# Kernel tuning notes

Measured on AMD Instinct MI355X. Metric: run time of the kernel, lower is better.

## Reference

```python
import jax, jax.numpy as jnp
import numpy as np

H, KV, D, HID = 32, 8, 128, 4096
B, S = 1, 2048
ROPE_THETA = 10000.0


def setup_inputs() -> dict:
    key = jax.random.key(0)
    ks = jax.random.split(key, 5)
    std = 0.02
    return {
        "x": jax.random.normal(ks[0], (B, S, HID), jnp.float32),
        "Wq": jax.random.normal(ks[1], (H * D, HID), jnp.float32) * std,
        "Wk": jax.random.normal(ks[2], (KV * D, HID), jnp.float32) * std,
        "Wv": jax.random.normal(ks[3], (KV * D, HID), jnp.float32) * std,
        "Wo": jax.random.normal(ks[4], (HID, H * D), jnp.float32) * std,
    }


def _rope_cos_sin(seq_len, dim, dtype):
    inv_freq = 1.0 / (ROPE_THETA ** (jnp.arange(0, dim, 2, dtype=jnp.float32) / dim))
    t = jnp.arange(seq_len, dtype=jnp.float32)
    freqs = jnp.einsum("s,d->sd", t, inv_freq)          # [S, D/2]
    emb = jnp.concatenate([freqs, freqs], axis=-1)        # [S, D]
    return jnp.cos(emb).astype(dtype), jnp.sin(emb).astype(dtype)


def _rotate_half(x):
    x1, x2 = jnp.split(x, 2, axis=-1)
    return jnp.concatenate([-x2, x1], axis=-1)


def reference(x, Wq, Wk, Wv, Wo):
    Bx, Sx, _ = x.shape
    q = (x @ Wq.T).reshape(Bx, Sx, H, D).transpose(0, 2, 1, 3)    # [B,H,S,D]
    k = (x @ Wk.T).reshape(Bx, Sx, KV, D).transpose(0, 2, 1, 3)   # [B,KV,S,D]
    v = (x @ Wv.T).reshape(Bx, Sx, KV, D).transpose(0, 2, 1, 3)

    cos, sin = _rope_cos_sin(Sx, D, x.dtype)                       # [S,D]
    q = q * cos + _rotate_half(q) * sin
    k = k * cos + _rotate_half(k) * sin

    rep = H // KV
    k = jnp.repeat(k, rep, axis=1)                                 # [B,H,S,D]
    v = jnp.repeat(v, rep, axis=1)

    scale = 1.0 / jnp.sqrt(jnp.asarray(D, x.dtype))
    scores = jnp.einsum("bhqd,bhkd->bhqk", q, k) * scale           # [B,H,S,S]
    causal = jnp.tril(jnp.ones((Sx, Sx), dtype=bool))
    scores = jnp.where(causal, scores, jnp.asarray(-1e30, x.dtype))
    attn = jax.nn.softmax(scores, axis=-1)
    out = jnp.einsum("bhqk,bhkd->bhqd", attn, v)                   # [B,H,S,D]
    out = out.transpose(0, 2, 1, 3).reshape(Bx, Sx, H * D)
    return out @ Wo.T
```

## Files before the change

kernel.cpp:

```cpp
#include <hip/hip_runtime.h>

typedef unsigned short u16;
typedef unsigned int u32;

using f32x4  = __attribute__((ext_vector_type(4))) float;
using f32x16 = __attribute__((ext_vector_type(16))) float;
using bf16x8 = __attribute__((ext_vector_type(8))) __bf16;

#define S_LEN 2048
#define HID_DIM 4096
#define NH 32
#define NKV 8
#define HD 128
#define QKVN 6144

__device__ __forceinline__ u16 f2b(float f) {
  union { float f; u32 u; } v; v.f = f;
  u32 r = (v.u + 0x7FFFu + ((v.u >> 16) & 1u)) >> 16;
  return (u16)r;
}
__device__ __forceinline__ float b2f(u16 b) {
  union { u32 u; float f; } v; v.u = ((u32)b) << 16;
  return v.f;
}

__device__ __forceinline__ u32 cvtpk_bf16(float lo, float hi) {
  u32 r;
  asm("v_cvt_pk_bf16_f32 %0, %1, %2" : "=v"(r) : "v"(lo), "v"(hi));
  return r;
}
__device__ __forceinline__ void plane_swap(u32& a, u32& b) {
  asm volatile("v_permlane32_swap_b32 %0, %1" : "+v"(a), "+v"(b));
}

#define AS1 __attribute__((address_space(1)))
#define AS3 __attribute__((address_space(3)))
__device__ __forceinline__ void gl_lds16(const u16* g, u16* l) {
  __builtin_amdgcn_global_load_lds((const AS1 u32*)g, (AS3 u32*)l, 16, 0, 0);
}

#define SBAR  __builtin_amdgcn_s_barrier()
#define SCHED0 __builtin_amdgcn_sched_barrier(0)
#define LGKM0 do { asm volatile("s_waitcnt lgkmcnt(0)" ::: "memory"); } while (0)
#define PRIO1 __builtin_amdgcn_s_setprio(1)
#define PRIO0 __builtin_amdgcn_s_setprio(0)

template <int N> __device__ __forceinline__ void waitv() {
  if constexpr (N == 0)      asm volatile("s_waitcnt vmcnt(0)" ::: "memory");
  else if constexpr (N == 6) asm volatile("s_waitcnt vmcnt(6)" ::: "memory");
  else if constexpr (N == 7) asm volatile("s_waitcnt vmcnt(7)" ::: "memory");
  else                       asm volatile("s_waitcnt vmcnt(0)" ::: "memory");
  SCHED0;
}

__global__ void cast_kernel(const float* __restrict__ src, u16* __restrict__ dst, int n4) {
  int i = blockIdx.x * blockDim.x + threadIdx.x;
  int stride = gridDim.x * blockDim.x;
  for (; i < n4; i += stride) {
    float4 v = ((const float4*)src)[i];
    uint2 o;
    o.x = (u32)f2b(v.x) | ((u32)f2b(v.y) << 16);
    o.y = (u32)f2b(v.z) | ((u32)f2b(v.w) << 16);
    ((uint2*)dst)[i] = o;
  }
}

#define STAGE(DST, SRC, CH, LDK)                                   \
  _Pragma("unroll") for (int c = 0; c < (CH); ++c) {               \
    int d_ = c * 8192 + tid * 16;                                  \
    int rw_ = d_ >> 7;                                             \
    int cb_ = (d_ & 127) ^ ((rw_ & 7) << 4);                       \
    gl_lds16((SRC) + (size_t)rw_ * (LDK) + (cb_ >> 1), (DST) + (d_ >> 1)); \
  }


#define RDA(ABUF, MLO, KS)                                                    \
  _Pragma("unroll") for (int mm = 0; mm < 4; ++mm)                            \
    af[(MLO) + mm][KS] = *(const bf16x8*)((const char*)(ABUF) +               \
      (wmo + ((MLO) + mm) * 16 + lr) * 128 + (((((KS) << 2) | lg) ^ lr7) << 4));

#define RDB(BBUF, KS)                                                         \
  _Pragma("unroll") for (int nn = 0; nn < NF; ++nn)                           \
    bfr[nn][KS] = *(const bf16x8*)((const char*)(BBUF) +                      \
      (wno + nn * 16 + lr) * 128 + (((((KS) << 2) | lg) ^ lr7) << 4));

#define MFMA_Q(MLO, KS)                                                       \
  _Pragma("unroll") for (int mm = 0; mm < 4; ++mm)                            \
  _Pragma("unroll") for (int nn = 0; nn < NF; ++nn)                           \
    acc[(MLO) + mm][nn] = __builtin_amdgcn_mfma_f32_16x16x32_bf16(            \
        af[(MLO) + mm][KS], bfr[nn][KS], acc[(MLO) + mm][nn], 0, 0, 0);

template <int BN, int WN, int CBF>
__global__ __launch_bounds__(512, 2) void gemm8p(
    const u16* __restrict__ A, const u16* __restrict__ B, void* __restrict__ Cout,
    int M, int N, int K)
{
  constexpr int BM = 256;
  constexpr int NF = WN / 16;
  constexpr int LA = BM / 64;
  constexpr int LB = BN / 64;
  constexpr int LT = LA + LB;
  extern __shared__ __align__(16) u16 smem[];
  u16* const As0 = smem;
  u16* const Bs0 = smem + 2 * BM * 64;

  const int tid  = threadIdx.x;
  const int lane = tid & 63;
  const int wave = tid >> 6;
  const int lr  = lane & 15;
  const int lg  = lane >> 4;
  const int lr7 = lane & 7;

  const int nbx = N / BN;
  const int bid = blockIdx.x;
  const int cpx = gridDim.x >> 3;
  const int swz = (bid & 7) * cpx + (bid >> 3);
  const int bm = (swz / nbx) * BM;
  const int bn = (swz % nbx) * BN;
  const int wmo = (wave >> 2) * 128;
  const int wno = (wave & 3) * WN;

  const int NT = K >> 6;

  f32x4 acc[8][NF] = {};
  bf16x8 af[8][2], bfr[NF][2];

  const u16* aP = A + (size_t)bm * K;
  const u16* bP = B + (size_t)bn * K;

  STAGE(As0,           aP,      LA, K);
  STAGE(Bs0,           bP,      LB, K);
  STAGE(As0 + BM * 64, aP + 64, LA, K);
  STAGE(Bs0 + BN * 64, bP + 64, LB, K);
  waitv<LT>();
  SBAR; SCHED0;

  for (int t = 0; t < NT; ++t) {
    const int buf = t & 1;
    const u16* ab = As0 + buf * (BM * 64);
    const u16* bb = Bs0 + buf * (BN * 64);
    const bool st = (t + 2 < NT);

    RDA(ab, 0, 0); RDA(ab, 4, 0); RDB(bb, 0);
    MFMA_Q(0, 0); MFMA_Q(4, 0);
    RDA(ab, 0, 1); RDA(ab, 4, 1); RDB(bb, 1);
    MFMA_Q(0, 1); MFMA_Q(4, 1);

    LGKM0;
    SCHED0;
    SBAR;
    if (st) {
      STAGE(As0 + buf * (BM * 64), aP + (size_t)(t + 2) * 64, LA, K);
      STAGE(Bs0 + buf * (BN * 64), bP + (size_t)(t + 2) * 64, LB, K);
    }
    if (t + 1 < NT) {
      if (st) waitv<LT>(); else waitv<0>();
    }
    SBAR; SCHED0;
  }

#pragma unroll
  for (int m = 0; m < 8; ++m)
#pragma unroll
    for (int j = 0; j < 4; ++j) {
      int row = bm + wmo + m * 16 + lg * 4 + j;
      size_t base = (size_t)row * N + bn + wno + lr;
      if constexpr (CBF) {
        u16* C = (u16*)Cout;
#pragma unroll
        for (int nn = 0; nn < NF; ++nn) C[base + nn * 16] = f2b(acc[m][nn][j]);
      } else {
        float* C = (float*)Cout;
#pragma unroll
        for (int nn = 0; nn < NF; ++nn) C[base + nn * 16] = acc[m][nn][j];
      }
    }
}

__global__ void rope_qk(const u16* __restrict__ qkv, u16* __restrict__ dst,
                        int col_off, float scale, int frag) {
  int idx = blockIdx.x * blockDim.x + threadIdx.x;
  int i = idx & 63;
  int s = (idx >> 6) & (S_LEN - 1);
  int h = idx >> 17;
  const u16* row = qkv + (size_t)s * QKVN + col_off + h * HD;
  float a = b2f(row[i]);
  float b = b2f(row[i + 64]);
  float invf = __expf(-(float)i * 0.14391156831212787f);
  float f = (float)s * invf;
  float sn, cs;
  sincosf(f, &sn, &cs);
  float o1 = (a * cs - b * sn) * scale;
  float o2 = (b * cs + a * sn) * scale;
  if (frag) {
    int qt = h * 64 + (s >> 5);
    int qq = s & 31;
    int i2 = i + 64;
    dst[((qt * 8 + (i  >> 4)) * 2 + ((i  >> 3) & 1)) * 256 + qq * 8 + (i  & 7)] = f2b(o1);
    dst[((qt * 8 + (i2 >> 4)) * 2 + ((i2 >> 3) & 1)) * 256 + qq * 8 + (i2 & 7)] = f2b(o2);
  } else {
    u16* orow = dst + ((size_t)h * S_LEN + s) * HD;
    orow[i]      = f2b(o1);
    orow[i + 64] = f2b(o2);
  }
}

__global__ __launch_bounds__(256) void vf_pack(const u16* __restrict__ qkv,
                                               u16* __restrict__ VF) {
  __shared__ u16 vlds[32][136];
  const int bid = blockIdx.x;
  const int kv = bid >> 6, t = bid & 63;
  const int tid = threadIdx.x;
  const int r = tid >> 3, d0 = (tid & 7) * 16;
  const u16* src = qkv + (size_t)(t * 32 + r) * QKVN + 5120 + kv * HD + d0;
  *(bf16x8*)&vlds[r][d0]     = *(const bf16x8*)src;
  *(bf16x8*)&vlds[r][d0 + 8] = *(const bf16x8*)(src + 8);
  __syncthreads();
  u16* outt = VF + (size_t)bid * 4096;
#pragma unroll
  for (int g = 0; g < 2; ++g) {
    int G = tid + g * 256;
    int q = G & 31, dt = (G >> 5) & 3, hi2 = (G >> 7) & 1, kc = G >> 8;
    union { u16 u[8]; uint4 v; } o;
#pragma unroll
    for (int e = 0; e < 8; ++e)
      o.u[e] = vlds[kc * 16 + hi2 * 8 + e][dt * 32 + q];
    *(uint4*)&outt[G * 8] = o.v;
  }
}

__global__ __launch_bounds__(256, 2) void attn_fwd(
    const u16* __restrict__ QF,
    const u16* __restrict__ KF,
    const u16* __restrict__ VF,
    u16* __restrict__ Out)
{
  const int tid  = threadIdx.x;
  const int lane = tid & 63;
  const int wv   = tid >> 6;
  const int q31  = lane & 31;
  const int hi   = lane >> 5;
  const int bid  = blockIdx.x;
  const int kvh  = bid & 7;
  const int qi   = 63 - (bid >> 3);
  const int q0   = qi * 32;
  const int h    = kvh * 4 + wv;
  const int nt   = qi + 1;

  const u16* kbase = KF + (size_t)kvh * 64 * 4096 + hi * 256  + q31 * 8;
  const u16* vbase = VF + (size_t)kvh * 64 * 4096 + hi * 1024 + q31 * 8;

  bf16x8 qf[8];
  const u16* qfp = QF + (size_t)(h * 64 + qi) * 4096 + hi * 256 + q31 * 8;
#pragma unroll
  for (int dc = 0; dc < 8; ++dc)
    qf[dc] = *(const bf16x8*)(qfp + dc * 512);

  f32x16 o0 = {}, o1 = {}, o2 = {}, o3 = {};
  float m = -1e30f, lsum = 0.f;

  for (int t = 0; t < nt; ++t) {
    SBAR;

    bf16x8 kf[8];
    const u16* kfp = kbase + (size_t)t * 4096;
#pragma unroll
    for (int dc = 0; dc < 8; ++dc)
      kf[dc] = *(const bf16x8*)(kfp + dc * 512);

    bf16x8 vf[8];
    const u16* vfp = vbase + (size_t)t * 4096;
#pragma unroll
    for (int i = 0; i < 8; ++i)
      vf[i] = *(const bf16x8*)(vfp + (i & 1) * 2048 + (i >> 1) * 256);

    f32x16 st = {};
    PRIO1;
#pragma unroll
    for (int dc = 0; dc < 8; ++dc)
      st = __builtin_amdgcn_mfma_f32_32x32x16_bf16(kf[dc], qf[dc], st, 0, 0, 0);
    PRIO0;

    if (t == nt - 1) {
#pragma unroll
      for (int r = 0; r < 16; ++r) {
        int kk = (r & 3) + 8 * (r >> 2) + 4 * hi;
        if (kk > q31) st[r] = -1e30f;
      }
    }

    float a0 = fmaxf(st[0], st[1]),   a1 = fmaxf(st[2], st[3]);
    float a2 = fmaxf(st[4], st[5]),   a3 = fmaxf(st[6], st[7]);
    float a4 = fmaxf(st[8], st[9]),   a5 = fmaxf(st[10], st[11]);
    float a6 = fmaxf(st[12], st[13]), a7 = fmaxf(st[14], st[15]);
    a0 = fmaxf(a0, a1); a2 = fmaxf(a2, a3); a4 = fmaxf(a4, a5); a6 = fmaxf(a6, a7);
    float pmax = fmaxf(fmaxf(a0, a2), fmaxf(a4, a6));
    pmax = fmaxf(pmax, __shfl_xor(pmax, 32));

    if (__any(pmax > m + 8.f)) {
      float mn = fmaxf(m, pmax);
      float sf = exp2f(m - mn);
      m = mn;
      lsum *= sf;
#pragma unroll
      for (int r = 0; r < 16; ++r) { o0[r] *= sf; o1[r] *= sf; o2[r] *= sf; o3[r] *= sf; }
    }

    float ev[16];
#pragma unroll
    for (int r = 0; r < 16; ++r) ev[r] = exp2f(st[r] - m);
    float s0 = (ev[0] + ev[1]) + (ev[2] + ev[3]);
    float s1 = (ev[4] + ev[5]) + (ev[6] + ev[7]);
    float s2 = (ev[8] + ev[9]) + (ev[10] + ev[11]);
    float s3 = (ev[12] + ev[13]) + (ev[14] + ev[15]);
    float ps = (s0 + s1) + (s2 + s3);
    ps += __shfl_xor(ps, 32);
    lsum += ps;

    u32 c0 = cvtpk_bf16(ev[0],  ev[1]),  c1 = cvtpk_bf16(ev[2],  ev[3]);
    u32 c2 = cvtpk_bf16(ev[4],  ev[5]),  c3 = cvtpk_bf16(ev[6],  ev[7]);
    u32 c4 = cvtpk_bf16(ev[8],  ev[9]),  c5 = cvtpk_bf16(ev[10], ev[11]);
    u32 c6 = cvtpk_bf16(ev[12], ev[13]), c7 = cvtpk_bf16(ev[14], ev[15]);
    plane_swap(c0, c2);
    plane_swap(c1, c3);
    plane_swap(c4, c6);
    plane_swap(c5, c7);
    union { u32 u[4]; bf16x8 v; } pb0u, pb1u;
    pb0u.u[0] = c0; pb0u.u[1] = c1; pb0u.u[2] = c2; pb0u.u[3] = c3;
    pb1u.u[0] = c4; pb1u.u[1] = c5; pb1u.u[2] = c6; pb1u.u[3] = c7;

    PRIO1;
    o0 = __builtin_amdgcn_mfma_f32_32x32x16_bf16(vf[0], pb0u.v, o0, 0, 0, 0);
    o1 = __builtin_amdgcn_mfma_f32_32x32x16_bf16(vf[2], pb0u.v, o1, 0, 0, 0);
    o2 = __builtin_amdgcn_mfma_f32_32x32x16_bf16(vf[4], pb0u.v, o2, 0, 0, 0);
    o3 = __builtin_amdgcn_mfma_f32_32x32x16_bf16(vf[6], pb0u.v, o3, 0, 0, 0);
    o0 = __builtin_amdgcn_mfma_f32_32x32x16_bf16(vf[1], pb1u.v, o0, 0, 0, 0);
    o1 = __builtin_amdgcn_mfma_f32_32x32x16_bf16(vf[3], pb1u.v, o1, 0, 0, 0);
    o2 = __builtin_amdgcn_mfma_f32_32x32x16_bf16(vf[5], pb1u.v, o2, 0, 0, 0);
    o3 = __builtin_amdgcn_mfma_f32_32x32x16_bf16(vf[7], pb1u.v, o3, 0, 0, 0);
    PRIO0;
  }

  float inv = 1.0f / lsum;
  u16* orow = Out + (size_t)(q0 + q31) * (NH * HD) + h * HD;
#pragma unroll
  for (int dt = 0; dt < 4; ++dt) {
    const f32x16& oo = dt == 0 ? o0 : dt == 1 ? o1 : dt == 2 ? o2 : o3;
#pragma unroll
    for (int g = 0; g < 4; ++g) {
      ushort4 pk;
      pk.x = f2b(oo[g * 4 + 0] * inv);
      pk.y = f2b(oo[g * 4 + 1] * inv);
      pk.z = f2b(oo[g * 4 + 2] * inv);
      pk.w = f2b(oo[g * 4 + 3] * inv);
      *(ushort4*)&orow[dt * 32 + 8 * g + 4 * hi] = pk;
    }
  }
}

extern "C" void kernel_launch(void* const* d_in, const int* in_sizes, int n_in,
                              void* d_out, int out_size, void* d_ws, size_t ws_size,
                              hipStream_t stream) {
  const float* x  = (const float*)d_in[0];
  const float* Wq = (const float*)d_in[1];
  const float* Wk = (const float*)d_in[2];
  const float* Wv = (const float*)d_in[3];
  const float* Wo = (const float*)d_in[4];
  float* out = (float*)d_out;

  char* ws = (char*)d_ws;
  u16* xb   = (u16*)(ws);
  u16* wqkv = (u16*)(ws + (16ull << 20));
  u16* wo_b = (u16*)(ws + (64ull << 20));
  u16* qkvb = (u16*)(ws + (96ull << 20));
  u16* qb   = (u16*)(ws + (16ull << 20));
  u16* kfb  = (u16*)(ws + (32ull << 20));
  u16* vfb  = (u16*)(ws + (36ull << 20));
  u16* ao   = (u16*)(ws);

  const int smem_q = (256 + 192) * 256;
  const int smem_o = (256 + 128) * 256;
  hipFuncSetAttribute((const void*)&gemm8p<192, 48, 1>,
                      hipFuncAttributeMaxDynamicSharedMemorySize, smem_q);
  hipFuncSetAttribute((const void*)&gemm8p<128, 32, 0>,
                      hipFuncAttributeMaxDynamicSharedMemorySize, smem_o);

  cast_kernel<<<4096, 256, 0, stream>>>(x,  xb,   (2048 * 4096) / 4);
  cast_kernel<<<4096, 256, 0, stream>>>(Wq, wqkv, (4096 * 4096) / 4);
  cast_kernel<<<2048, 256, 0, stream>>>(Wk, wqkv + (size_t)4096 * 4096, (1024 * 4096) / 4);
  cast_kernel<<<2048, 256, 0, stream>>>(Wv, wqkv + (size_t)5120 * 4096, (1024 * 4096) / 4);
  cast_kernel<<<4096, 256, 0, stream>>>(Wo, wo_b, (4096 * 4096) / 4);

  gemm8p<192, 48, 1><<<256, 512, smem_q, stream>>>(xb, wqkv, qkvb, 2048, 6144, 4096);

  rope_qk<<<(32 * 2048 * 64) / 256, 256, 0, stream>>>(qkvb, qb,  0,    0.12751741f, 1);
  rope_qk<<<(8  * 2048 * 64) / 256, 256, 0, stream>>>(qkvb, kfb, 4096, 1.0f,        1);
  vf_pack<<<512, 256, 0, stream>>>(qkvb, vfb);

  attn_fwd<<<512, 256, 0, stream>>>(qb, kfb, vfb, ao);

  gemm8p<128, 32, 0><<<256, 512, smem_o, stream>>>(ao, wo_b, out, 2048, 4096, 4096);
}
```

Measured before the change: 315.9 us.

## Rewrite GEMM with 256-wide N tiles, interleaved staging, and fuse cast kernels

```diff
diff --git a/kernel.cpp b/kernel.cpp
--- a/kernel.cpp
+++ b/kernel.cpp
@@ -41,27 +41,43 @@
 
 #define SBAR  __builtin_amdgcn_s_barrier()
 #define SCHED0 __builtin_amdgcn_sched_barrier(0)
-#define LGKM0 do { asm volatile("s_waitcnt lgkmcnt(0)" ::: "memory"); } while (0)
+#define LGKM0 do { asm volatile("s_waitcnt lgkmcnt(0)" ::: "memory"); SCHED0; } while (0)
 #define PRIO1 __builtin_amdgcn_s_setprio(1)
 #define PRIO0 __builtin_amdgcn_s_setprio(0)
 
 template <int N> __device__ __forceinline__ void waitv() {
   if constexpr (N == 0)      asm volatile("s_waitcnt vmcnt(0)" ::: "memory");
+  else if constexpr (N == 4) asm volatile("s_waitcnt vmcnt(4)" ::: "memory");
   else if constexpr (N == 6) asm volatile("s_waitcnt vmcnt(6)" ::: "memory");
-  else if constexpr (N == 7) asm volatile("s_waitcnt vmcnt(7)" ::: "memory");
   else                       asm volatile("s_waitcnt vmcnt(0)" ::: "memory");
   SCHED0;
 }
 
-__global__ void cast_kernel(const float* __restrict__ src, u16* __restrict__ dst, int n4) {
+#define X4T 2097152
+#define Q4T 4194304
+#define K4T 1048576
+#define TOT4 (X4T + Q4T + K4T + K4T + Q4T)
+__global__ void cast_all(const float* __restrict__ x,  const float* __restrict__ wq,
+                         const float* __restrict__ wk, const float* __restrict__ wv,
+                         const float* __restrict__ wo,
+                         u16* __restrict__ xb, u16* __restrict__ wqkv,
+                         u16* __restrict__ wo_b) {
   int i = blockIdx.x * blockDim.x + threadIdx.x;
   int stride = gridDim.x * blockDim.x;
-  for (; i < n4; i += stride) {
-    float4 v = ((const float4*)src)[i];
+  for (; i < TOT4; i += stride) {
+    const float* src;
+    uint2* dst;
+    int off;
+    if (i < X4T)                     { src = x;  dst = (uint2*)xb;   off = i; }
+    else if (i < X4T + Q4T)          { src = wq; dst = (uint2*)wqkv; off = i - X4T; }
+    else if (i < X4T + Q4T + K4T)    { src = wk; dst = (uint2*)wqkv + Q4T; off = i - X4T - Q4T; }
+    else if (i < X4T + Q4T + 2*K4T)  { src = wv; dst = (uint2*)wqkv + Q4T + K4T; off = i - X4T - Q4T - K4T; }
+    else                             { src = wo; dst = (uint2*)wo_b; off = i - X4T - Q4T - 2*K4T; }
+    float4 v = ((const float4*)src)[off];
     uint2 o;
     o.x = (u32)f2b(v.x) | ((u32)f2b(v.y) << 16);
     o.y = (u32)f2b(v.z) | ((u32)f2b(v.w) << 16);
-    ((uint2*)dst)[i] = o;
+    dst[off] = o;
   }
 }
 
@@ -73,36 +89,36 @@
     gl_lds16((SRC) + (size_t)rw_ * (LDK) + (cb_ >> 1), (DST) + (d_ >> 1)); \
   }
 
-
-#define RDA(ABUF, MLO, KS)                                                    \
-  _Pragma("unroll") for (int mm = 0; mm < 4; ++mm)                            \
-    af[(MLO) + mm][KS] = *(const bf16x8*)((const char*)(ABUF) +               \
-      (wmo + ((MLO) + mm) * 16 + lr) * 128 + (((((KS) << 2) | lg) ^ lr7) << 4));
-
-#define RDB(BBUF, KS)                                                         \
-  _Pragma("unroll") for (int nn = 0; nn < NF; ++nn)                           \
-    bfr[nn][KS] = *(const bf16x8*)((const char*)(BBUF) +                      \
-      (wno + nn * 16 + lr) * 128 + (((((KS) << 2) | lg) ^ lr7) << 4));
-
-#define MFMA_Q(MLO, KS)                                                       \
-  _Pragma("unroll") for (int mm = 0; mm < 4; ++mm)                            \
-  _Pragma("unroll") for (int nn = 0; nn < NF; ++nn)                           \
-    acc[(MLO) + mm][nn] = __builtin_amdgcn_mfma_f32_16x16x32_bf16(            \
-        af[(MLO) + mm][KS], bfr[nn][KS], acc[(MLO) + mm][nn], 0, 0, 0);
-
-template <int BN, int WN, int CBF>
-__global__ __launch_bounds__(512, 2) void gemm8p(
+#define RB8(BB)                                                               \
+  _Pragma("unroll") for (int nn = 0; nn < 4; ++nn)                            \
+  _Pragma("unroll") for (int ks = 0; ks < 2; ++ks)                            \
+    bfr[nn][ks] = *(const bf16x8*)((const char*)(BB) +                        \
+      (wno + nn * 16 + lr) * 128 + ((((ks << 2) | lg) ^ lr7) << 4));
+
+#define RAQ(AB, Q)                                                            \
+  _Pragma("unroll") for (int j = 0; j < 2; ++j)                               \
+  _Pragma("unroll") for (int ks = 0; ks < 2; ++ks)                            \
+    af[j][ks] = *(const bf16x8*)((const char*)(AB) +                          \
+      (wmo + (Q) * 32 + j * 16 + lr) * 128 + ((((ks << 2) | lg) ^ lr7) << 4));
+
+#define MQ16(Q)                                                               \
+  _Pragma("unroll") for (int ks = 0; ks < 2; ++ks)                            \
+  _Pragma("unroll") for (int j = 0; j < 2; ++j)                               \
+  _Pragma("unroll") for (int nn = 0; nn < 4; ++nn)                            \
+    acc[(Q) * 2 + j][nn] = __builtin_amdgcn_mfma_f32_16x16x32_bf16(           \
+        af[j][ks], bfr[nn][ks], acc[(Q) * 2 + j][nn], 0, 0, 0);
+
+template <int BM, int CBF>
+__global__ __launch_bounds__(512, 2) void gemm_m2(
     const u16* __restrict__ A, const u16* __restrict__ B, void* __restrict__ Cout,
     int M, int N, int K)
 {
-  constexpr int BM = 256;
-  constexpr int NF = WN / 16;
+  constexpr int MF = BM / 32;
   constexpr int LA = BM / 64;
-  constexpr int LB = BN / 64;
-  constexpr int LT = LA + LB;
+  constexpr int ASZ = BM * 64;
   extern __shared__ __align__(16) u16 smem[];
-  u16* const As0 = smem;
-  u16* const Bs0 = smem + 2 * BM * 64;
+  u16* const As = smem;
+  u16* const Bs = smem + 2 * ASZ;
 
   const int tid  = threadIdx.x;
   const int lane = tid & 63;
@@ -111,56 +127,75 @@
   const int lg  = lane >> 4;
   const int lr7 = lane & 7;
 
-  const int nbx = N / BN;
+  const int nbx = N / 256;
   const int bid = blockIdx.x;
   const int cpx = gridDim.x >> 3;
   const int swz = (bid & 7) * cpx + (bid >> 3);
   const int bm = (swz / nbx) * BM;
-  const int bn = (swz % nbx) * BN;
-  const int wmo = (wave >> 2) * 128;
-  const int wno = (wave & 3) * WN;
+  const int bn = (swz % nbx) * 256;
+  const int wmo = (wave >> 2) * (BM / 2);
+  const int wno = (wave & 3) * 64;
 
   const int NT = K >> 6;
 
-  f32x4 acc[8][NF] = {};
-  bf16x8 af[8][2], bfr[NF][2];
+  f32x4 acc[MF][4] = {};
+  bf16x8 af[2][2], bfr[4][2];
 
   const u16* aP = A + (size_t)bm * K;
   const u16* bP = B + (size_t)bn * K;
 
-  STAGE(As0,           aP,      LA, K);
-  STAGE(Bs0,           bP,      LB, K);
-  STAGE(As0 + BM * 64, aP + 64, LA, K);
-  STAGE(Bs0 + BN * 64, bP + 64, LB, K);
-  waitv<LT>();
+  STAGE(As,          aP,      LA, K);
+  STAGE(Bs,          bP,      4,  K);
+  STAGE(Bs + 16384,  bP + 64, 4,  K);
+  waitv<4>();
   SBAR; SCHED0;
 
   for (int t = 0; t < NT; ++t) {
-    const int buf = t & 1;
-    const u16* ab = As0 + buf * (BM * 64);
-    const u16* bb = Bs0 + buf * (BN * 64);
-    const bool st = (t + 2 < NT);
-
-    RDA(ab, 0, 0); RDA(ab, 4, 0); RDB(bb, 0);
-    MFMA_Q(0, 0); MFMA_Q(4, 0);
-    RDA(ab, 0, 1); RDA(ab, 4, 1); RDB(bb, 1);
-    MFMA_Q(0, 1); MFMA_Q(4, 1);
-
-    LGKM0;
+    const int s = t & 1;
+    const int o = s ^ 1;
+    const u16* ab = As + s * ASZ;
+    const u16* bb = Bs + s * 16384;
+    const bool stA = (t + 1 < NT);
+    const bool stB = (t + 2 < NT);
+
+    RAQ(ab, 0); RB8(bb);
+    if (stA) { STAGE(As + o * ASZ, aP + (size_t)(t + 1) * 64, (MF == 8 ? 2 : LA), K); }
+    SCHED0; SBAR; LGKM0;
+    PRIO1; MQ16(0); PRIO0;
+    SBAR;
+
+    RAQ(ab, 1);
+    if constexpr (MF == 8) {
+      if (stA) { STAGE(As + o * ASZ + 8192, aP + (size_t)128 * K + (size_t)(t + 1) * 64, 2, K); }
+    } else {
+      if (stB) { STAGE(Bs + s * 16384, bP + (size_t)(t + 2) * 64, 4, K); }
+    }
+    SCHED0; SBAR; LGKM0;
+    PRIO1; MQ16(1); PRIO0;
+    if constexpr (MF == 4) {
+      if (stB) { waitv<4>(); } else if (stA) { waitv<0>(); }
+    }
+    SBAR;
+
+    if constexpr (MF == 8) {
+      RAQ(ab, 2);
+      if (stB) { STAGE(Bs + s * 16384, bP + (size_t)(t + 2) * 64, 2, K); }
+      SCHED0; SBAR; LGKM0;
+      PRIO1; MQ16(2); PRIO0;
+      SBAR;
+
+      RAQ(ab, 3);
+      if (stB) { STAGE(Bs + s * 16384 + 8192, bP + (size_t)128 * K + (size_t)(t + 2) * 64, 2, K); }
+      SCHED0; SBAR; LGKM0;
+      PRIO1; MQ16(3); PRIO0;
+      if (stB) { waitv<4>(); } else if (stA) { waitv<0>(); }
+      SBAR;
+    }
     SCHED0;
-    SBAR;
-    if (st) {
-      STAGE(As0 + buf * (BM * 64), aP + (size_t)(t + 2) * 64, LA, K);
-      STAGE(Bs0 + buf * (BN * 64), bP + (size_t)(t + 2) * 64, LB, K);
-    }
-    if (t + 1 < NT) {
-      if (st) waitv<LT>(); else waitv<0>();
-    }
-    SBAR; SCHED0;
-  }
-
-#pragma unroll
-  for (int m = 0; m < 8; ++m)
+  }
+
+#pragma unroll
+  for (int m = 0; m < MF; ++m)
 #pragma unroll
     for (int j = 0; j < 4; ++j) {
       int row = bm + wmo + m * 16 + lg * 4 + j;
@@ -168,11 +203,11 @@
       if constexpr (CBF) {
         u16* C = (u16*)Cout;
 #pragma unroll
-        for (int nn = 0; nn < NF; ++nn) C[base + nn * 16] = f2b(acc[m][nn][j]);
+        for (int nn = 0; nn < 4; ++nn) C[base + nn * 16] = f2b(acc[m][nn][j]);
       } else {
         float* C = (float*)Cout;
 #pragma unroll
-        for (int nn = 0; nn < NF; ++nn) C[base + nn * 16] = acc[m][nn][j];
+        for (int nn = 0; nn < 4; ++nn) C[base + nn * 16] = acc[m][nn][j];
       }
     }
 }
@@ -378,20 +413,16 @@
   u16* vfb  = (u16*)(ws + (36ull << 20));
   u16* ao   = (u16*)(ws);
 
-  const int smem_q = (256 + 192) * 256;
-  const int smem_o = (256 + 128) * 256;
-  hipFuncSetAttribute((const void*)&gemm8p<192, 48, 1>,
+  const int smem_q = 2 * (256 * 64 + 256 * 64) * 2;
+  const int smem_o = 2 * (128 * 64 + 256 * 64) * 2;
+  hipFuncSetAttribute((const void*)&gemm_m2<256, 1>,
                       hipFuncAttributeMaxDynamicSharedMemorySize, smem_q);
-  hipFuncSetAttribute((const void*)&gemm8p<128, 32, 0>,
+  hipFuncSetAttribute((const void*)&gemm_m2<128, 0>,
                       hipFuncAttributeMaxDynamicSharedMemorySize, smem_o);
 
-  cast_kernel<<<4096, 256, 0, stream>>>(x,  xb,   (2048 * 4096) / 4);
-  cast_kernel<<<4096, 256, 0, stream>>>(Wq, wqkv, (4096 * 4096) / 4);
-  cast_kernel<<<2048, 256, 0, stream>>>(Wk, wqkv + (size_t)4096 * 4096, (1024 * 4096) / 4);
-  cast_kernel<<<2048, 256, 0, stream>>>(Wv, wqkv + (size_t)5120 * 4096, (1024 * 4096) / 4);
-  cast_kernel<<<4096, 256, 0, stream>>>(Wo, wo_b, (4096 * 4096) / 4);
-
-  gemm8p<192, 48, 1><<<256, 512, smem_q, stream>>>(xb, wqkv, qkvb, 2048, 6144, 4096);
+  cast_all<<<4096, 256, 0, stream>>>(x, Wq, Wk, Wv, Wo, xb, wqkv, wo_b);
+
+  gemm_m2<256, 1><<<192, 512, smem_q, stream>>>(xb, wqkv, qkvb, 2048, 6144, 4096);
 
   rope_qk<<<(32 * 2048 * 64) / 256, 256, 0, stream>>>(qkvb, qb,  0,    0.12751741f, 1);
   rope_qk<<<(8  * 2048 * 64) / 256, 256, 0, stream>>>(qkvb, kfb, 4096, 1.0f,        1);
@@ -399,5 +430,5 @@
 
   attn_fwd<<<512, 256, 0, stream>>>(qb, kfb, vfb, ao);
 
-  gemm8p<128, 32, 0><<<256, 512, smem_o, stream>>>(ao, wo_b, out, 2048, 4096, 4096);
-}
+  gemm_m2<128, 0><<<256, 512, smem_o, stream>>>(ao, wo_b, out, 2048, 4096, 4096);
+}
```

After: 322.0 us. Within noise of the previous version (+1.9%).
